# Optimization experiments

Measured on AMD Instinct MI355X. Metric: run time of the kernel, lower is better.

Reference implementation:

```python
import jax, jax.numpy as jnp
import numpy as np

I_SZ, H_SZ, M_SZ, D_SZ, T_LEN = 256, 512, 16384, 256, 128


def setup_inputs() -> dict:
    key = jax.random.key(0)
    ks = iter(jax.random.split(key, 48))

    def rn(shape, s=0.05):
        return jax.random.normal(next(ks), shape, dtype=jnp.float32) * s

    Hd, D = H_SZ, D_SZ
    inp = {
        "inputs": rn((T_LEN, 1, I_SZ), 1.0),
        "memory0": rn((M_SZ, D), 0.01),            # register_buffer: randn*0.01
        "read_w0": jnp.zeros((M_SZ,), jnp.float32),
        "write_w0": jnp.zeros((M_SZ,), jnp.float32),
        "W_ih": rn((4 * Hd, I_SZ + D)),             # LSTM input->gates (i,f,g,o)
        "W_hh": rn((4 * Hd, Hd)),
        "b_ih": jnp.zeros((4 * Hd,), jnp.float32),
        "b_hh": jnp.zeros((4 * Hd,), jnp.float32),
        "Wo": rn((I_SZ, Hd + D)),                   # output_layer
        "bo": jnp.zeros((I_SZ,), jnp.float32),
    }
    for p in ("r", "w"):  # read head / write head addressing params
        inp[p + "_Wk"] = rn((D, Hd)); inp[p + "_bk"] = jnp.zeros((D,), jnp.float32)
        inp[p + "_Wb"] = rn((1, Hd)); inp[p + "_bb"] = jnp.zeros((1,), jnp.float32)
        inp[p + "_Wg"] = rn((1, Hd)); inp[p + "_bg"] = jnp.zeros((1,), jnp.float32)
        inp[p + "_Ws"] = rn((3, Hd)); inp[p + "_bs"] = jnp.zeros((3,), jnp.float32)
        inp[p + "_Wp"] = rn((1, Hd)); inp[p + "_bp"] = jnp.zeros((1,), jnp.float32)
    inp["w_We"] = rn((D, Hd)); inp["w_be"] = jnp.zeros((D,), jnp.float32)  # erase
    inp["w_Wa"] = rn((D, Hd)); inp["w_ba"] = jnp.zeros((D,), jnp.float32)  # add
    return inp


def _attend(co, mem, prev_w, Wk, bk, Wb, bb, Wg, bg, Ws, bs, Wp, bp):
    # co: (1,H), mem: (M,D), prev_w: (M,) -> (M,)
    key = co @ Wk.T + bk                                   # (1,D)
    beta = jax.nn.softplus(co @ Wb.T + bb)                 # (1,1) key strength
    kn = key / jnp.maximum(jnp.linalg.norm(key, axis=-1, keepdims=True), 1e-12)
    mn = mem / jnp.maximum(jnp.linalg.norm(mem, axis=-1, keepdims=True), 1e-12)
    cw = jax.nn.softmax(beta * (kn @ mn.T), axis=-1)       # (1,M) content weights
    g = jax.nn.sigmoid(co @ Wg.T + bg)                     # interpolation gate
    gw = g * cw + (1.0 - g) * prev_w[None, :]
    s = jax.nn.softmax(co @ Ws.T + bs, axis=-1)            # (1,3) shift kernel
    shifted = (s[:, 0:1] * jnp.roll(gw, -1, axis=-1)
               + s[:, 1:2] * gw
               + s[:, 2:3] * jnp.roll(gw, 1, axis=-1))
    gamma = jax.nn.softplus(co @ Wp.T + bp) + 1.0          # sharpening >= 1
    w = shifted ** gamma
    return (w / (w.sum(-1, keepdims=True) + 1e-8))[0]


def reference(inputs, memory0, read_w0, write_w0, W_ih, W_hh, b_ih, b_hh, Wo, bo,
              r_Wk, r_bk, r_Wb, r_bb, r_Wg, r_bg, r_Ws, r_bs, r_Wp, r_bp,
              w_Wk, w_bk, w_Wb, w_bb, w_Wg, w_bg, w_Ws, w_bs, w_Wp, w_bp,
              w_We, w_be, w_Wa, w_ba):
    H = W_hh.shape[1]

    def step(carry, x_t):
        mem, rw, ww, h, c = carry
        read_vec = rw @ mem                                  # (D,) read old memory
        ci = jnp.concatenate([x_t[0], read_vec])[None, :]    # (1, I+D)
        gates = ci @ W_ih.T + b_ih + h @ W_hh.T + b_hh       # (1, 4H)
        i_, f_, g_, o_ = jnp.split(gates, 4, axis=-1)
        c_new = jax.nn.sigmoid(f_) * c + jax.nn.sigmoid(i_) * jnp.tanh(g_)
        h_new = jax.nn.sigmoid(o_) * jnp.tanh(c_new)
        co = h_new                                           # controller output (1,H)
        ww_new = _attend(co, mem, ww, w_Wk, w_bk, w_Wb, w_bb, w_Wg, w_bg, w_Ws, w_bs, w_Wp, w_bp)
        erase = jax.nn.sigmoid(co @ w_We.T + w_be)[0]        # (D,)
        add = (co @ w_Wa.T + w_ba)[0]                        # (D,)
        mem_new = mem * (1.0 - ww_new[:, None] * erase[None, :]) + ww_new[:, None] * add[None, :]
        rw_new = _attend(co, mem_new, rw, r_Wk, r_bk, r_Wb, r_bb, r_Wg, r_bg, r_Ws, r_bs, r_Wp, r_bp)
        out = jnp.concatenate([co[0], read_vec])[None, :] @ Wo.T + bo  # (1, I)
        return (mem_new, rw_new, ww_new, h_new, c_new), out

    init = (memory0, read_w0, write_w0,
            jnp.zeros((1, H), inputs.dtype), jnp.zeros((1, H), inputs.dtype))
    _, outs = jax.lax.scan(step, init, inputs)               # (T,1,I)
    return outs
```

## Files before the change

kernel.cpp:

```cpp
#include <hip/hip_runtime.h>
#include <math.h>


#define NBLK 128
#define NTHR 512
#define Msz  16384
#define Dsz  256
#define Hsz  512
#define Isz  256
#define Tlen 128
#define RPB  128
#define NG   16

#define CNT1 (1ull << 48)

struct Params { const float* in[34]; float* out; float* ws; };

__device__ __forceinline__ float wred64(float v){
#pragma unroll
  for (int o = 32; o > 0; o >>= 1) v += __shfl_xor(v, o, 64);
  return v;
}
__device__ __forceinline__ float wred32(float v){
#pragma unroll
  for (int o = 16; o > 0; o >>= 1) v += __shfl_xor(v, o, 32);
  return v;
}
__device__ __forceinline__ float qsum4(float v){
  v += __uint_as_float(__builtin_amdgcn_mov_dpp(__float_as_uint(v), 0xB1, 0xF, 0xF, true));
  v += __uint_as_float(__builtin_amdgcn_mov_dpp(__float_as_uint(v), 0x4E, 0xF, 0xF, true));
  return v;
}
__device__ __forceinline__ float sigm(float x){ return 1.f / (1.f + __expf(-x)); }
__device__ __forceinline__ float softplusf(float x){ return (x > 20.f) ? x : log1pf(__expf(x)); }

__device__ __forceinline__ void gstore(float* p, float v){
  __hip_atomic_store(p, v, __ATOMIC_RELAXED, __HIP_MEMORY_SCOPE_AGENT);
}
__device__ __forceinline__ float gload(const float* p){
  return __hip_atomic_load(p, __ATOMIC_RELAXED, __HIP_MEMORY_SCOPE_AGENT);
}
__device__ __forceinline__ void gstore64(unsigned long long* p, unsigned long long v){
  __hip_atomic_store(p, v, __ATOMIC_RELAXED, __HIP_MEMORY_SCOPE_AGENT);
}
__device__ __forceinline__ unsigned long long gload64(const unsigned long long* p){
  return __hip_atomic_load(p, __ATOMIC_RELAXED, __HIP_MEMORY_SCOPE_AGENT);
}
__device__ __forceinline__ void lbar(){
  __builtin_amdgcn_s_waitcnt(0xC07F);
  __builtin_amdgcn_s_barrier();
}
__device__ __forceinline__ float pollw(const unsigned long long* p, unsigned want){
  unsigned long long k;
  do { k = gload64(p); } while ((int)((unsigned)(k >> 32) - want) < 0);
  return __uint_as_float((unsigned)k);
}
__device__ __forceinline__ unsigned long long fxpack(float v){
  return CNT1 + (unsigned long long)((double)v * 4294967296.0);
}

__global__ void __launch_bounds__(NTHR, 1)
ntm_kernel(Params P)
{
  const int b   = blockIdx.x;
  const int tid = threadIdx.x;
  const int wv  = tid >> 6;
  const int ln  = tid & 63;

  const float* inputs  = P.in[0];
  const float* mem0    = P.in[1];
  const float* read_w0 = P.in[2];
  const float* write_w0= P.in[3];
  const float* W_ih = P.in[4];
  const float* W_hh = P.in[5];
  const float* b_ih = P.in[6];
  const float* b_hh = P.in[7];
  const float* Wo   = P.in[8];
  const float* bo   = P.in[9];
  const float* r_Wk = P.in[10]; const float* r_bk = P.in[11];
  const float* r_Wb = P.in[12]; const float* r_bb = P.in[13];
  const float* r_Wg = P.in[14]; const float* r_bg = P.in[15];
  const float* r_Ws = P.in[16]; const float* r_bs = P.in[17];
  const float* r_Wp = P.in[18]; const float* r_bp = P.in[19];
  const float* w_Wk = P.in[20]; const float* w_bk = P.in[21];
  const float* w_Wb = P.in[22]; const float* w_bb = P.in[23];
  const float* w_Wg = P.in[24]; const float* w_bg = P.in[25];
  const float* w_Ws = P.in[26]; const float* w_bs = P.in[27];
  const float* w_Wp = P.in[28]; const float* w_bp = P.in[29];
  const float* w_We = P.in[30]; const float* w_be = P.in[31];
  const float* w_Wa = P.in[32]; const float* w_ba = P.in[33];
  float* out = P.out;

  float* ws = P.ws;
  float* PA = ws;
  float* PB = ws + 4096;
  unsigned long long* U = (unsigned long long*)(ws + 8192);
  unsigned long long* hpub = U;
  unsigned long long* ppub = U + 1024;
  unsigned long long* wEF  = U + 2320;
  unsigned long long* wPF  = wEF + 128;
  unsigned long long* wEL  = wPF + 128;
  unsigned long long* wPL  = wEL + 128;
  unsigned long long* rEF  = wPL + 128;
  unsigned long long* rPF  = rEF + 128;
  unsigned long long* rEL  = rPF + 128;
  unsigned long long* rPL  = rEL + 128;
  unsigned long long* redD = U + 3344;
  unsigned long long* redF = redD + 8 * Tlen;
  unsigned long long* redH = redF + 8 * Tlen;
  unsigned long long* redJ = redH + 8 * Tlen;
  unsigned long long* redI = redJ + 8 * Tlen;
  float* Pbuf[2] = { PA, PB };
  const int slot = b & 7;

  __shared__ float s_mem[RPB * Dsz];
  __shared__ float s_co[Hsz];
  __shared__ float s_a[256];
  __shared__ float s_er[256], s_ad[256], s_kr[256];
  __shared__ float s_rv[256];
  __shared__ float s_norm[RPB];
  __shared__ float s_e[RPB];
  __shared__ float s_bw[RPB];
  __shared__ float s_rw[RPB];
  __shared__ float s_ww[RPB];
  __shared__ float s_A1[RPB], s_A2[RPB], s_B1[RPB], s_B0[RPB];
  __shared__ float s_dot[RPB];
  __shared__ float s_red[8];
  __shared__ float s_lg[16];
  __shared__ float s_scal[16];
  __shared__ float s_w2[2];
  __shared__ float s_cst[4];
  __shared__ float s_bd[4];
  __shared__ float s_pub;
  __shared__ float s_gval;

  auto redWait8 = [&](unsigned long long* base, int t)->float{
    if (tid == 0){
      unsigned long long k0,k1,k2,k3,k4,k5,k6,k7;
      for (;;){
        k0 = gload64(base + 0*Tlen + t); k1 = gload64(base + 1*Tlen + t);
        k2 = gload64(base + 2*Tlen + t); k3 = gload64(base + 3*Tlen + t);
        k4 = gload64(base + 4*Tlen + t); k5 = gload64(base + 5*Tlen + t);
        k6 = gload64(base + 6*Tlen + t); k7 = gload64(base + 7*Tlen + t);
        unsigned c = (unsigned)(k0>>48) + (unsigned)(k1>>48)
                   + (unsigned)(k2>>48) + (unsigned)(k3>>48)
                   + (unsigned)(k4>>48) + (unsigned)(k5>>48)
                   + (unsigned)(k6>>48) + (unsigned)(k7>>48);
        if (c >= (unsigned)NBLK) break;
      }
      const unsigned long long m = 0xFFFFFFFFFFFFull;
      unsigned long long s = (k0&m)+(k1&m)+(k2&m)+(k3&m)+(k4&m)+(k5&m)+(k6&m)+(k7&m);
      s_gval = (float)((double)s * (1.0 / 4294967296.0));
    }
    lbar();
    return s_gval;
  };
  auto redWait1 = [&](unsigned long long* p)->float{
    if (tid == 0){
      unsigned long long k;
      do { k = gload64(p); } while ((unsigned)(k >> 48) < (unsigned)NBLK);
      s_gval = (float)((double)(k & 0xFFFFFFFFFFFFull) * (1.0 / 4294967296.0));
    }
    lbar();
    return s_gval;
  };

  auto bred512 = [&](float v)->float{
    v = wred64(v);
    lbar();
    if (ln == 0) s_red[wv] = v;
    lbar();
    return s_red[0] + s_red[1] + s_red[2] + s_red[3]
         + s_red[4] + s_red[5] + s_red[6] + s_red[7];
  };

  auto shiftSharpen = [&](int si, float* s_prevw, float S, unsigned long long* slotp){
    float g     = sigm(s_scal[si + 1]);
    float gamma = softplusf(s_scal[si + 2]) + 1.f;
    float a0 = s_scal[si + 3], a1 = s_scal[si + 4], a2 = s_scal[si + 5];
    float mx = fmaxf(a0, fmaxf(a1, a2));
    float e0 = __expf(a0 - mx), e1 = __expf(a1 - mx), e2 = __expf(a2 - mx);
    float idn = 1.f / (e0 + e1 + e2);
    float s0 = e0 * idn, s1 = e1 * idn, s2 = e2 * idn;
    float invS = 1.f / S;
    float w = 0.f;
    if (tid < RPB){
      float gc = g * invS, gp = 1.f - g;
      float em = s_e[tid],  pm = s_prevw[tid];
      float e1n = (tid < RPB-1) ? s_e[tid+1]     : s_bd[0];
      float p1n = (tid < RPB-1) ? s_prevw[tid+1] : s_bd[1];
      float e2n = (tid > 0)     ? s_e[tid-1]     : s_bd[2];
      float p2n = (tid > 0)     ? s_prevw[tid-1] : s_bd[3];
      float gwm = gc * em  + gp * pm;
      float gw1 = gc * e1n + gp * p1n;
      float gw2 = gc * e2n + gp * p2n;
      float sh = s0 * gw1 + s1 * gwm + s2 * gw2;
      w = powf(sh, gamma);
      s_bw[tid] = w;
    }
    float tot = wred64(w);
    if (ln == 0 && wv < 2) s_w2[wv] = tot;
    lbar();
    if (tid == 0){
      float T2 = s_w2[0] + s_w2[1];
      s_pub = T2;
      if (slotp) atomicAdd(slotp, fxpack(T2));
    }
  };

  auto gemvXH = [&]()->float{
    int dd = tid >> 5, l = tid & 31;
    int r = (dd >> 2) * Hsz + (b << 2) + (dd & 3);
    const float* wi = W_ih + (size_t)r * (Isz + Dsz);
    const float* wh = W_hh + (size_t)r * Hsz;
    float acc = 0.f;
#pragma unroll
    for (int it = 0; it < 2; ++it){
      int k = it * 128 + l * 4;
      float4 a = *(const float4*)(wi + k);
      float4 x = *(const float4*)(&s_a[k]);
      acc += a.x*x.x + a.y*x.y + a.z*x.z + a.w*x.w;
    }
#pragma unroll
    for (int it = 0; it < 4; ++it){
      int k = it * 128 + l * 4;
      float4 hw = *(const float4*)(wh + k);
      float4 hv = *(const float4*)(&s_co[k]);
      acc += hw.x*hv.x + hw.y*hv.y + hw.z*hv.z + hw.w*hv.w;
    }
    return acc;
  };

  float Srcarry = 1.f;
  float accxh   = 0.f;

  {
    if (b < NG && tid < 256){ gstore(&PA[b*256 + tid], 0.f); gstore(&PB[b*256 + tid], 0.f); }
    if (tid < RPB){
      s_rw[tid] = read_w0[b * RPB + tid];
      s_ww[tid] = write_w0[b * RPB + tid];
    }
    if (tid < 4) s_cst[tid] = 0.f;
    s_co[tid] = 0.f;
    __syncthreads();
    if (tid == 0) atomicAdd(redI + 0, CNT1);
    redWait1(redI + 0);
  }

  {
#pragma unroll 1
    for (int it = 0; it < 16; ++it){
      int ml = it * 8 + wv;
      int m  = b * RPB + ml;
      float4 v = *(const float4*)(mem0 + (size_t)m * Dsz + ln * 4);
      *(float4*)(&s_mem[ml * Dsz + ln * 4]) = v;
      float n2 = wred64(v.x*v.x + v.y*v.y + v.z*v.z + v.w*v.w);
      if (ln == 0) s_norm[ml] = sqrtf(n2);
    }
    lbar();
    int col = tid & 255, half = tid >> 8;
    float acc = 0.f;
#pragma unroll 1
    for (int j = half * 64; j < half * 64 + 64; ++j) acc += s_rw[j] * s_mem[j * Dsz + col];
    if (half == 0) s_a[col] = acc;
    lbar();
    if (half == 1) atomicAdd(&PB[(b & (NG-1)) * 256 + col], acc + s_a[col]);
    __syncthreads();
    if (tid < 256) s_a[tid] = inputs[tid];
    if (tid == 0) atomicAdd(redI + 1, CNT1);
    lbar();
    accxh = gemvXH();
    redWait1(redI + 1);
  }

  for (int t = 0; t < Tlen; ++t){
    const unsigned TT = (unsigned)(t + 3);
    const unsigned long long tg = (unsigned long long)TT << 32;
    float* Pcur = Pbuf[t & 1];
    float* Prd  = Pbuf[(t + 1) & 1];

    {
      float SrDiv = (t == 0) ? 1.f : (Srcarry + 1e-8f);
      if (t > 0 && tid < RPB) s_rw[tid] = s_bw[tid] / SrDiv;
      if (tid < 256){
        float rvv = 0.f;
#pragma unroll
        for (int p = 0; p < NG; ++p) rvv += gload(&Prd[p * 256 + tid]);
        s_rv[tid] = rvv / SrDiv;
      }
      lbar();
      int dd = tid >> 5, l = tid & 31;
      int r = (dd >> 2) * Hsz + (b << 2) + (dd & 3);
      const float* wi = W_ih + (size_t)r * (Isz + Dsz) + Isz;
      float acc = accxh;
#pragma unroll
      for (int it = 0; it < 2; ++it){
        int k = it * 128 + l * 4;
        float4 a = *(const float4*)(wi + k);
        float4 x = *(const float4*)(&s_rv[k]);
        acc += a.x*x.x + a.y*x.y + a.z*x.z + a.w*x.w;
      }
      acc = wred32(acc);
      if (l == 0) s_lg[dd] = acc + b_ih[r] + b_hh[r];
      lbar();
      if (tid < 4){
        float iv = s_lg[tid], fv = s_lg[4 + tid], gv = s_lg[8 + tid], ov = s_lg[12 + tid];
        float cn = sigm(fv) * s_cst[tid] + sigm(iv) * tanhf(gv);
        s_cst[tid] = cn;
        float hn = sigm(ov) * tanhf(cn);
        gstore64(&hpub[(size_t)b * 8 + tid], tg | (unsigned long long)__float_as_uint(hn));
      }
    }

    {
      s_co[tid] = pollw(&hpub[(size_t)(tid >> 2) * 8 + (tid & 3)], TT);
      lbar();
#pragma unroll
      for (int qi = 0; qi < 2; ++qi){
        int q = qi * 8 + wv;
        int pslot = q * 128 + b;
        if (pslot < 1292){
          const float* Wrow = nullptr; float bias = 0.f; int len = 512;
          int mode = 0;
          if (pslot < 256){ Wrow = w_Wk + (size_t)pslot * Hsz; bias = w_bk[pslot]; }
          else if (pslot < 512){ int i = pslot - 256; Wrow = w_We + (size_t)i * Hsz; bias = w_be[i]; mode = 1; }
          else if (pslot < 768){ int i = pslot - 512; Wrow = w_Wa + (size_t)i * Hsz; bias = w_ba[i]; }
          else if (pslot < 1024){ int i = pslot - 768; Wrow = r_Wk + (size_t)i * Hsz; bias = r_bk[i]; }
          else if (pslot < 1280){ int i = pslot - 1024; Wrow = Wo + (size_t)i * (Hsz + Dsz); bias = bo[i]; len = 768; mode = 2; }
          else {
            int i = pslot - 1280;
            int ii = (i >= 6) ? i - 6 : i;
            bool rh = (i >= 6);
            const float *Wt, *bt; int row = 0;
            if (ii == 0){ Wt = rh ? r_Wb : w_Wb; bt = rh ? r_bb : w_bb; }
            else if (ii == 1){ Wt = rh ? r_Wg : w_Wg; bt = rh ? r_bg : w_bg; }
            else if (ii == 2){ Wt = rh ? r_Wp : w_Wp; bt = rh ? r_bp : w_bp; }
            else { Wt = rh ? r_Ws : w_Ws; bt = rh ? r_bs : w_bs; row = ii - 3; }
            Wrow = Wt + (size_t)row * Hsz; bias = bt[row];
          }
          float acc = 0.f;
          if (len == 512){
            int k = ln * 8;
            float4 a0 = *(const float4*)(Wrow + k);
            float4 a1 = *(const float4*)(Wrow + k + 4);
            float4 c0 = *(const float4*)(&s_co[k]);
            float4 c1 = *(const float4*)(&s_co[k + 4]);
            acc = a0.x*c0.x + a0.y*c0.y + a0.z*c0.z + a0.w*c0.w
                + a1.x*c1.x + a1.y*c1.y + a1.z*c1.z + a1.w*c1.w;
          } else {
            int k = ln * 4;
            float4 w0 = *(const float4*)(Wrow + k);
            float4 w1 = *(const float4*)(Wrow + 256 + k);
            float4 w2 = *(const float4*)(Wrow + 512 + k);
            float4 c0 = *(const float4*)(&s_co[k]);
            float4 c1 = *(const float4*)(&s_co[256 + k]);
            float4 r0 = *(const float4*)(&s_rv[k]);
            acc = w0.x*c0.x + w0.y*c0.y + w0.z*c0.z + w0.w*c0.w
                + w1.x*c1.x + w1.y*c1.y + w1.z*c1.z + w1.w*c1.w
                + w2.x*r0.x + w2.y*r0.y + w2.z*r0.z + w2.w*r0.w;
          }
          acc = wred64(acc);
          if (ln == 0){
            float v = acc + bias;
            if (mode == 1) v = sigm(v);
            if (mode == 2) out[(size_t)t * Isz + (pslot - 1024)] = v;
            else gstore64(&ppub[pslot], tg | (unsigned long long)__float_as_uint(v));
          }
        }
      }
    }

    if (t == Tlen - 1) break;

    float betaR = 0.f, invbkR = 0.f;

    {
      float* Pnx = Pbuf[(t + 1) & 1];
      if (b < NG && tid < 256) gstore(&Pnx[b * 256 + tid], 0.f);
      if (tid < 256) s_a[tid] = pollw(&ppub[tid], TT);
      else if (tid < 268) s_scal[tid - 256] = pollw(&ppub[1280 + (tid - 256)], TT);
      lbar();
      float nk2 = bred512((tid < 256) ? s_a[tid] * s_a[tid] : 0.f);
      float beta  = softplusf(s_scal[0]);
      float invbk = beta / fmaxf(sqrtf(nk2), 1e-12f);
      int row = tid >> 2, q = tid & 3;
      const float* mrow = &s_mem[row * Dsz];
      float d = 0.f;
#pragma unroll
      for (int k = 0; k < 16; ++k){
        int c = (q + 4 * ((k + row) & 15)) * 4;
        float4 mv = *(const float4*)(mrow + c);
        float4 kv = *(const float4*)(&s_a[c]);
        d += mv.x*kv.x + mv.y*kv.y + mv.z*kv.z + mv.w*kv.w;
      }
      d = qsum4(d);
      if (q == 0) s_dot[row] = d;
      lbar();
      float e = 0.f;
      if (tid < RPB){
        float score = s_dot[tid] * invbk / fmaxf(s_norm[tid], 1e-12f);
        e = __expf(score - beta);
        s_e[tid] = e;
      }
      float tot = wred64(e);
      if (ln == 0 && wv < 2) s_w2[wv] = tot;
      lbar();
      if (tid == 0){
        float T = s_w2[0] + s_w2[1];
        gstore64(&wEF[b], tg | (unsigned long long)__float_as_uint(s_e[0]));
        gstore64(&wPF[b], tg | (unsigned long long)__float_as_uint(s_ww[0]));
        gstore64(&wEL[b], tg | (unsigned long long)__float_as_uint(s_e[RPB-1]));
        gstore64(&wPL[b], tg | (unsigned long long)__float_as_uint(s_ww[RPB-1]));
        atomicAdd(redD + slot * Tlen + t, fxpack(T));
      }
    }

    {
      if (tid < 256) s_er[tid] = pollw(&ppub[256 + tid], TT);
      else           s_ad[tid - 256] = pollw(&ppub[512 + (tid - 256)], TT);
      if (tid < 256) s_kr[tid] = pollw(&ppub[768 + tid], TT);
      float nk2r = bred512((tid < 256) ? s_kr[tid] * s_kr[tid] : 0.f);
      betaR  = softplusf(s_scal[6]);
      invbkR = betaR / fmaxf(sqrtf(nk2r), 1e-12f);
      int row = tid >> 2, q = tid & 3;
      const float* mrow = &s_mem[row * Dsz];
      float mq = 0.f, qq = 0.f, qk = 0.f, mk = 0.f;
#pragma unroll
      for (int k = 0; k < 16; ++k){
        int c = (q + 4 * ((k + row) & 15)) * 4;
        float4 mv = *(const float4*)(mrow + c);
        float4 er = *(const float4*)(&s_er[c]);
        float4 ad = *(const float4*)(&s_ad[c]);
        float4 kr = *(const float4*)(&s_kr[c]);
        float qx = ad.x - mv.x * er.x;
        float qy = ad.y - mv.y * er.y;
        float qz = ad.z - mv.z * er.z;
        float qw = ad.w - mv.w * er.w;
        mq += mv.x*qx + mv.y*qy + mv.z*qz + mv.w*qw;
        qq += qx*qx + qy*qy + qz*qz + qw*qw;
        qk += qx*kr.x + qy*kr.y + qz*kr.z + qw*kr.w;
        mk += mv.x*kr.x + mv.y*kr.y + mv.z*kr.z + mv.w*kr.w;
      }
      mq = qsum4(mq); qq = qsum4(qq); qk = qsum4(qk); mk = qsum4(mk);
      if (q == 0){ s_A1[row] = 2.f*mq; s_A2[row] = qq; s_B1[row] = qk; s_B0[row] = mk; }
    }

    {
      if (wv == 0 && ln < 4){
        const unsigned long long* bp = (ln == 0) ? &wEF[(b + 1) & (NBLK-1)]
                               : (ln == 1) ? &wPF[(b + 1) & (NBLK-1)]
                               : (ln == 2) ? &wEL[(b - 1) & (NBLK-1)]
                                           : &wPL[(b - 1) & (NBLK-1)];
        s_bd[ln] = pollw(bp, TT);
      }
      float S_w = redWait8(redD, t);
      shiftSharpen(0, s_ww, S_w, redF + slot * Tlen + t);
    }

    {
      float Sw = redWait8(redF, t);
      float invSw = 1.f / (Sw + 1e-8f);
      float4 er4 = *(const float4*)(&s_er[ln * 4]);
      float4 ad4 = *(const float4*)(&s_ad[ln * 4]);
      float e = 0.f;
      if (tid < RPB){
        float wwm = s_bw[tid] * invSw;
        s_ww[tid] = wwm;
        float A0 = s_norm[tid] * s_norm[tid];
        float n2 = fmaf(wwm, fmaf(wwm, s_A2[tid], s_A1[tid]), A0);
        float dt = fmaf(wwm, s_B1[tid], s_B0[tid]);
        float nr = sqrtf(fmaxf(n2, 0.f));
        s_norm[tid] = nr;
        float score = dt * invbkR / fmaxf(nr, 1e-12f);
        e = __expf(score - betaR);
        s_e[tid] = e;
      }
      float tot = wred64(e);
      if (ln == 0 && wv < 2) s_w2[wv] = tot;
      lbar();
      if (tid == 0){
        float T2 = s_w2[0] + s_w2[1];
        gstore64(&rEF[b], tg | (unsigned long long)__float_as_uint(s_e[0]));
        gstore64(&rPF[b], tg | (unsigned long long)__float_as_uint(s_rw[0]));
        gstore64(&rEL[b], tg | (unsigned long long)__float_as_uint(s_e[RPB-1]));
        gstore64(&rPL[b], tg | (unsigned long long)__float_as_uint(s_rw[RPB-1]));
        atomicAdd(redH + slot * Tlen + t, fxpack(T2));
      }
#pragma unroll 1
      for (int it = 0; it < 16; ++it){
        int ml = it * 8 + wv;
        int off = ml * Dsz + ln * 4;
        float wwm = s_bw[ml] * invSw;
        float4 mv = *(const float4*)(&s_mem[off]);
        float4 nv;
        nv.x = fmaf(wwm, ad4.x - mv.x * er4.x, mv.x);
        nv.y = fmaf(wwm, ad4.y - mv.y * er4.y, mv.y);
        nv.z = fmaf(wwm, ad4.z - mv.z * er4.z, mv.z);
        nv.w = fmaf(wwm, ad4.w - mv.w * er4.w, mv.w);
        *(float4*)(&s_mem[off]) = nv;
      }
    }

    {
      if (wv == 0 && ln < 4){
        const unsigned long long* bp = (ln == 0) ? &rEF[(b + 1) & (NBLK-1)]
                               : (ln == 1) ? &rPF[(b + 1) & (NBLK-1)]
                               : (ln == 2) ? &rEL[(b - 1) & (NBLK-1)]
                                           : &rPL[(b - 1) & (NBLK-1)];
        s_bd[ln] = pollw(bp, TT);
      }
      float S_r = redWait8(redH, t);
      shiftSharpen(6, s_rw, S_r, nullptr);
      lbar();
      int col = tid & 255, half = tid >> 8;
      float acc = 0.f;
#pragma unroll 1
      for (int j = half * 64; j < half * 64 + 64; ++j) acc += s_bw[j] * s_mem[j * Dsz + col];
      if (half == 0) s_a[col] = acc;
      lbar();
      if (half == 1) atomicAdd(&Pcur[(b & (NG-1)) * 256 + col], acc + s_a[col]);
      __syncthreads();
      if (tid == 0) atomicAdd(redJ + slot * Tlen + t, fxpack(s_pub));
      if (tid < 256) s_a[tid] = inputs[(size_t)(t + 1) * Isz + tid];
      lbar();
      accxh = gemvXH();
      Srcarry = redWait8(redJ, t);
    }
  }
}

extern "C" void kernel_launch(void* const* d_in, const int* in_sizes, int n_in,
                              void* d_out, int out_size, void* d_ws, size_t ws_size,
                              hipStream_t stream)
{
  (void)in_sizes; (void)out_size;
  if (n_in < 34) return;
  if (ws_size < (size_t)98304) return;
  Params P;
  for (int i = 0; i < 34; ++i) P.in[i] = (const float*)d_in[i];
  P.out = (float*)d_out;
  P.ws  = (float*)d_ws;
  hipLaunchKernelGGL(ntm_kernel, dim3(NBLK), dim3(NTHR), 0, stream, P);
}
```

Baseline: 3.606 ms.

## Overlap LSTM gate GEMV with addressing and globalize key-norm reductions

Splits the gate GEMV into an input part computed early from global inputs and a hidden part split across two phases, so the work overlaps with waits instead of sitting on the critical path at step end. Key norms for the write and read heads are now accumulated via global fixed-point atomics by the producer blocks rather than recomputed with block-wide reductions. Work assignment per wave is reordered so the key/read-key producing rows are handled first. This adds more global atomics and polling and extra hpub reads, and relies on the fixed-point precision of the squared-norm sums.

```diff
diff --git a/kernel.cpp b/kernel.cpp
--- a/kernel.cpp
+++ b/kernel.cpp
@@ -110,6 +110,8 @@
   unsigned long long* redH = redF + 8 * Tlen;
   unsigned long long* redJ = redH + 8 * Tlen;
   unsigned long long* redI = redJ + 8 * Tlen;
+  unsigned long long* redK  = redI + 2;
+  unsigned long long* redKr = redK + Tlen;
   float* Pbuf[2] = { PA, PB };
   const int slot = b & 7;
 
@@ -125,7 +127,6 @@
   __shared__ float s_ww[RPB];
   __shared__ float s_A1[RPB], s_A2[RPB], s_B1[RPB], s_B0[RPB];
   __shared__ float s_dot[RPB];
-  __shared__ float s_red[8];
   __shared__ float s_lg[16];
   __shared__ float s_scal[16];
   __shared__ float s_w2[2];
@@ -155,23 +156,14 @@
     lbar();
     return s_gval;
   };
-  auto redWait1 = [&](unsigned long long* p)->float{
+  auto redWaitC = [&](unsigned long long* p, unsigned target)->float{
     if (tid == 0){
       unsigned long long k;
-      do { k = gload64(p); } while ((unsigned)(k >> 48) < (unsigned)NBLK);
+      do { k = gload64(p); } while ((unsigned)(k >> 48) < target);
       s_gval = (float)((double)(k & 0xFFFFFFFFFFFFull) * (1.0 / 4294967296.0));
     }
     lbar();
     return s_gval;
-  };
-
-  auto bred512 = [&](float v)->float{
-    v = wred64(v);
-    lbar();
-    if (ln == 0) s_red[wv] = v;
-    lbar();
-    return s_red[0] + s_red[1] + s_red[2] + s_red[3]
-         + s_red[4] + s_red[5] + s_red[6] + s_red[7];
   };
 
   auto shiftSharpen = [&](int si, float* s_prevw, float S, unsigned long long* slotp){
@@ -208,21 +200,26 @@
     }
   };
 
-  auto gemvXH = [&]()->float{
+  auto xpart = [&](const float* xn)->float{
     int dd = tid >> 5, l = tid & 31;
     int r = (dd >> 2) * Hsz + (b << 2) + (dd & 3);
     const float* wi = W_ih + (size_t)r * (Isz + Dsz);
-    const float* wh = W_hh + (size_t)r * Hsz;
     float acc = 0.f;
 #pragma unroll
     for (int it = 0; it < 2; ++it){
       int k = it * 128 + l * 4;
       float4 a = *(const float4*)(wi + k);
-      float4 x = *(const float4*)(&s_a[k]);
+      float4 x = *(const float4*)(xn + k);
       acc += a.x*x.x + a.y*x.y + a.z*x.z + a.w*x.w;
     }
-#pragma unroll
-    for (int it = 0; it < 4; ++it){
+    return acc;
+  };
+  auto gemvHpart = [&](int i0, int i1)->float{
+    int dd = tid >> 5, l = tid & 31;
+    int r = (dd >> 2) * Hsz + (b << 2) + (dd & 3);
+    const float* wh = W_hh + (size_t)r * Hsz;
+    float acc = 0.f;
+    for (int it = i0; it < i1; ++it){
       int k = it * 128 + l * 4;
       float4 hw = *(const float4*)(wh + k);
       float4 hv = *(const float4*)(&s_co[k]);
@@ -232,7 +229,7 @@
   };
 
   float Srcarry = 1.f;
-  float accxh   = 0.f;
+  float accxh = 0.f, accX = 0.f, accH = 0.f;
 
   {
     if (b < NG && tid < 256){ gstore(&PA[b*256 + tid], 0.f); gstore(&PB[b*256 + tid], 0.f); }
@@ -244,7 +241,7 @@
     s_co[tid] = 0.f;
     __syncthreads();
     if (tid == 0) atomicAdd(redI + 0, CNT1);
-    redWait1(redI + 0);
+    redWaitC(redI + 0, NBLK);
   }
 
   {
@@ -266,11 +263,9 @@
     lbar();
     if (half == 1) atomicAdd(&PB[(b & (NG-1)) * 256 + col], acc + s_a[col]);
     __syncthreads();
-    if (tid < 256) s_a[tid] = inputs[tid];
     if (tid == 0) atomicAdd(redI + 1, CNT1);
-    lbar();
-    accxh = gemvXH();
-    redWait1(redI + 1);
+    accxh = xpart(inputs);
+    redWaitC(redI + 1, NBLK);
   }
 
   for (int t = 0; t < Tlen; ++t){
@@ -315,9 +310,12 @@
     {
       s_co[tid] = pollw(&hpub[(size_t)(tid >> 2) * 8 + (tid & 3)], TT);
       lbar();
+      const int QB0[8] = {0,1,10,2,3,4,5,6};
+      const int QB1[8] = {7,8,9,-1,-1,-1,-1,-1};
 #pragma unroll
       for (int qi = 0; qi < 2; ++qi){
-        int q = qi * 8 + wv;
+        int q = (qi == 0) ? QB0[wv] : QB1[wv];
+        if (q < 0) continue;
         int pslot = q * 128 + b;
         if (pslot < 1292){
           const float* Wrow = nullptr; float bias = 0.f; int len = 512;
@@ -365,6 +363,8 @@
             if (mode == 1) v = sigm(v);
             if (mode == 2) out[(size_t)t * Isz + (pslot - 1024)] = v;
             else gstore64(&ppub[pslot], tg | (unsigned long long)__float_as_uint(v));
+            if (q <= 1)                 atomicAdd(redK  + t, fxpack(v * v));
+            else if (q == 6 || q == 7)  atomicAdd(redKr + t, fxpack(v * v));
           }
         }
       }
@@ -375,12 +375,12 @@
     float betaR = 0.f, invbkR = 0.f;
 
     {
+      accX = xpart(inputs + (size_t)(t + 1) * Isz);
       float* Pnx = Pbuf[(t + 1) & 1];
       if (b < NG && tid < 256) gstore(&Pnx[b * 256 + tid], 0.f);
       if (tid < 256) s_a[tid] = pollw(&ppub[tid], TT);
       else if (tid < 268) s_scal[tid - 256] = pollw(&ppub[1280 + (tid - 256)], TT);
-      lbar();
-      float nk2 = bred512((tid < 256) ? s_a[tid] * s_a[tid] : 0.f);
+      float nk2 = redWaitC(redK + t, 256);
       float beta  = softplusf(s_scal[0]);
       float invbk = beta / fmaxf(sqrtf(nk2), 1e-12f);
       int row = tid >> 2, q = tid & 3;
@@ -419,7 +419,7 @@
       if (tid < 256) s_er[tid] = pollw(&ppub[256 + tid], TT);
       else           s_ad[tid - 256] = pollw(&ppub[512 + (tid - 256)], TT);
       if (tid < 256) s_kr[tid] = pollw(&ppub[768 + tid], TT);
-      float nk2r = bred512((tid < 256) ? s_kr[tid] * s_kr[tid] : 0.f);
+      float nk2r = redWaitC(redKr + t, 256);
       betaR  = softplusf(s_scal[6]);
       invbkR = betaR / fmaxf(sqrtf(nk2r), 1e-12f);
       int row = tid >> 2, q = tid & 3;
@@ -455,6 +455,9 @@
       }
       float S_w = redWait8(redD, t);
       shiftSharpen(0, s_ww, S_w, redF + slot * Tlen + t);
+      s_co[tid] = pollw(&hpub[(size_t)(tid >> 2) * 8 + (tid & 3)], TT);
+      lbar();
+      accH = gemvHpart(0, 2);
     }
 
     {
@@ -521,9 +524,7 @@
       if (half == 1) atomicAdd(&Pcur[(b & (NG-1)) * 256 + col], acc + s_a[col]);
       __syncthreads();
       if (tid == 0) atomicAdd(redJ + slot * Tlen + t, fxpack(s_pub));
-      if (tid < 256) s_a[tid] = inputs[(size_t)(t + 1) * Isz + tid];
-      lbar();
-      accxh = gemvXH();
+      accxh = accX + accH + gemvHpart(2, 4);
       Srcarry = redWait8(redJ, t);
     }
   }
```

Measured after the change: 3.645 ms. About the same (+1.1%).
